# Performance work log

Hardware: AMD Instinct MI355X
Metric: run time of the kernel (lower is better)

Reference implementation:

```python
import jax, jax.numpy as jnp
import numpy as np

T = 128        # number of timesteps (init arg T)
LEN_M = 32     # causal window length (init arg len_M)
N = 8192       # nodes
F = 64         # features per node


def setup_inputs() -> dict:
    key = jax.random.key(0)
    k1, k2, k3 = jax.random.split(key, 3)
    X = jax.random.normal(k1, (T, N, F), dtype=jnp.float32)
    # M_pad[r] holds the length-(r+1) parameter M[str(r+1)] in its first r+1 slots
    # (padding is masked out before softmax, so its values are irrelevant).
    M_pad = jax.random.normal(k2, (LEN_M, LEN_M), dtype=jnp.float32)
    # M_big[j] corresponds to parameter key str(LEN_M+1+j); keys LEN_M+1..T-1 are
    # used by rows LEN_M+1..T-1 (row LEN_M reuses M[str(LEN_M)] = M_pad[-1], per the source).
    M_big = jax.random.normal(k3, (T - LEN_M - 1, LEN_M), dtype=jnp.float32)
    return {"X": X, "M_pad": M_pad, "M_big": M_big}


def _band_weights(M_pad, M_big):
    """Build the [T, T] causal banded mixing matrix with per-row softmax weights."""
    cols = jnp.arange(LEN_M)
    # rows 0..LEN_M-1: softmax over the growing prefix window of length row+1
    prefix_mask = cols[None, :] <= jnp.arange(LEN_M)[:, None]            # [LEN_M, LEN_M]
    w_small = jax.nn.softmax(jnp.where(prefix_mask, M_pad, -jnp.inf), axis=1)
    # rows LEN_M..T-1 use key str(row): row==LEN_M reuses M_pad[-1], rest use M_big
    logits_big = jnp.concatenate([M_pad[LEN_M - 1:LEN_M], M_big], axis=0)  # [T-LEN_M, LEN_M]
    w_big = jax.nn.softmax(logits_big, axis=1)
    W = jnp.zeros((T, T), dtype=M_pad.dtype)
    W = W.at[:LEN_M, :LEN_M].set(w_small)  # w_small is zero outside the prefix window
    rows = jnp.arange(LEN_M, T)
    cidx = (rows - LEN_M + 1)[:, None] + cols[None, :]  # sliding window cols per row
    W = W.at[rows[:, None], cidx].set(w_big)
    return W


def reference(X, M_pad, M_big):
    W = _band_weights(M_pad, M_big)          # [T, T] banded
    data = X.reshape(T, -1)                  # [T, N*F]
    out = W @ data                           # causal windowed weighted sum, all rows at once
    return out.reshape(X.shape)
```

## Files before the change

kernel.cpp:

```cpp
#include <hip/hip_runtime.h>
#include <math.h>

#define T_    128
#define LENM  32
#define NCOL  (8192 * 64)

typedef float f4_t __attribute__((ext_vector_type(4)));

__global__ void build_w_kernel(const float* __restrict__ M_pad,
                               const float* __restrict__ M_big,
                               float* __restrict__ Wc) {
    int t = threadIdx.x;
    if (t >= T_) return;
    const float* src;
    int len, joff;
    if (t < LENM)       { src = M_pad + t * LENM;              len = t + 1; joff = LENM - 1 - t; }
    else if (t == LENM) { src = M_pad + (LENM - 1) * LENM;     len = LENM;  joff = 0; }
    else                { src = M_big + (t - LENM - 1) * LENM; len = LENM;  joff = 0; }

    float m = -3.4e38f;
    for (int j = 0; j < len; ++j) m = fmaxf(m, src[j]);
    float e[LENM];
    float s = 0.f;
    for (int j = 0; j < len; ++j) { e[j] = expf(src[j] - m); s += e[j]; }
    float inv = 1.f / s;
    for (int j = 0; j < LENM; ++j) Wc[t * LENM + j] = 0.f;
    for (int j = 0; j < len; ++j)  Wc[t * LENM + joff + j] = e[j] * inv;
}

template<int R>
__device__ __forceinline__ void step(const f4_t* __restrict__ xp,
                                     f4_t* __restrict__ op,
                                     const f4_t* w4,
                                     f4_t (&A)[LENM], f4_t (&B)[LENM]) {
    constexpr int K     = R / LENM;
    constexpr int i_    = R % LENM;
    constexpr int jmin_ = (R < LENM) ? (LENM - 1 - i_) : 0;
    f4_t (&CUR)[LENM] = (K & 1) ? B : A;
    f4_t (&PRV)[LENM] = (K & 1) ? A : B;
    const size_t rs = NCOL / 4;

    if constexpr (R + 8 < T_) {
        f4_t ld = xp[(size_t)(R + 8) * rs];
        if constexpr (i_ < LENM - 8) CUR[i_ + 8] = ld;
        else                         PRV[i_ - (LENM - 8)] = ld;
    }

    f4_t acc; acc.x = 0.f; acc.y = 0.f; acc.z = 0.f; acc.w = 0.f;
#pragma unroll
    for (int q = 0; q < 8; ++q) {
        if (q * 4 + 3 >= jmin_) {
            f4_t w = w4[R * 8 + q];
#pragma unroll
            for (int m = 0; m < 4; ++m) {
                const int j = q * 4 + m;
                if (j >= jmin_) {
                    f4_t xv = (j < LENM - 1 - i_) ? PRV[i_ + 1 + j]
                                                  : CUR[i_ + j - (LENM - 1)];
                    float wm = (m == 0) ? w.x : (m == 1) ? w.y
                             : (m == 2) ? w.z : w.w;
                    acc.x = fmaf(wm, xv.x, acc.x);
                    acc.y = fmaf(wm, xv.y, acc.y);
                    acc.z = fmaf(wm, xv.z, acc.z);
                    acc.w = fmaf(wm, xv.w, acc.w);
                }
            }
        }
    }
    __builtin_nontemporal_store(acc, &op[(size_t)R * rs]);
}

template<int R>
__device__ __forceinline__ void run_steps(const f4_t* __restrict__ xp,
                                          f4_t* __restrict__ op,
                                          const f4_t* w4,
                                          f4_t (&A)[LENM], f4_t (&B)[LENM]) {
    if constexpr (R < T_) {
        step<R>(xp, op, w4, A, B);
        run_steps<R + 1>(xp, op, w4, A, B);
    }
}

__global__ __launch_bounds__(256, 2) void band_mix_kernel(
    const float* __restrict__ X,
    const float* __restrict__ Wc,
    float* __restrict__ out) {
    __shared__ f4_t w4[T_ * LENM / 4];
    for (int i = threadIdx.x; i < T_ * LENM / 4; i += 256)
        w4[i] = reinterpret_cast<const f4_t*>(Wc)[i];
    __syncthreads();

    const int c = (blockIdx.x * 256 + threadIdx.x) * 4;
    const f4_t* xp = reinterpret_cast<const f4_t*>(X + c);
    f4_t* op = reinterpret_cast<f4_t*>(out + c);
    const size_t rs = NCOL / 4;

    f4_t A[LENM], B[LENM];
#pragma unroll
    for (int i = 0; i < 8; ++i) A[i] = xp[(size_t)i * rs];

    run_steps<0>(xp, op, w4, A, B);
}

extern "C" void kernel_launch(void* const* d_in, const int* in_sizes, int n_in,
                              void* d_out, int out_size, void* d_ws, size_t ws_size,
                              hipStream_t stream) {
    const float* X     = (const float*)d_in[0];
    const float* M_pad = (const float*)d_in[1];
    const float* M_big = (const float*)d_in[2];
    float* out = (float*)d_out;
    float* Wc  = (float*)d_ws;

    build_w_kernel<<<1, 128, 0, stream>>>(M_pad, M_big, Wc);
    band_mix_kernel<<<NCOL / 4 / 256, 256, 0, stream>>>(X, Wc, out);
}
```

Baseline: 95.32 us.

## Replace double-bank row buffer with 48-slot ring and grouped prefetch

Replaces the two 32-entry register banks with a single 48-slot ring buffer indexed by row modulo 48. Rows are loaded in groups of eight, one group ahead of the group being computed, and a scheduling barrier separates the loads from the FMA work. This keeps more loads in flight and cuts the register footprint of the window. The ring stays large enough that no row still needed is overwritten, but the compiler may reorder or spill registers differently.

After: 106.6 us. 1.12x slower.

```diff
diff --git a/kernel.cpp b/kernel.cpp
--- a/kernel.cpp
+++ b/kernel.cpp
@@ -1,9 +1,11 @@
 #include <hip/hip_runtime.h>
 #include <math.h>
 
-#define T_    128
-#define LENM  32
-#define NCOL  (8192 * 64)
+#define T_     128
+#define LENM   32
+#define NCOL   (8192 * 64)
+#define WSLOTS 48
+#define GRP    8
 
 typedef float f4_t __attribute__((ext_vector_type(4)));
 
@@ -28,35 +30,37 @@
     for (int j = 0; j < len; ++j)  Wc[t * LENM + joff + j] = e[j] * inv;
 }
 
-template<int R>
-__device__ __forceinline__ void step(const f4_t* __restrict__ xp,
-                                     f4_t* __restrict__ op,
-                                     const f4_t* w4,
-                                     f4_t (&A)[LENM], f4_t (&B)[LENM]) {
-    constexpr int K     = R / LENM;
-    constexpr int i_    = R % LENM;
-    constexpr int jmin_ = (R < LENM) ? (LENM - 1 - i_) : 0;
-    f4_t (&CUR)[LENM] = (K & 1) ? B : A;
-    f4_t (&PRV)[LENM] = (K & 1) ? A : B;
-    const size_t rs = NCOL / 4;
 
-    if constexpr (R + 8 < T_) {
-        f4_t ld = xp[(size_t)(R + 8) * rs];
-        if constexpr (i_ < LENM - 8) CUR[i_ + 8] = ld;
-        else                         PRV[i_ - (LENM - 8)] = ld;
+template<int ROW>
+__device__ __forceinline__ void load_row(const f4_t* __restrict__ xp,
+                                         f4_t (&WIN)[WSLOTS]) {
+    WIN[ROW % WSLOTS] = xp[(size_t)ROW * (NCOL / 4)];
+}
+
+template<int R0, int CNT>
+__device__ __forceinline__ void load_rows(const f4_t* __restrict__ xp,
+                                          f4_t (&WIN)[WSLOTS]) {
+    if constexpr (CNT > 0) {
+        load_row<R0>(xp, WIN);
+        load_rows<R0 + 1, CNT - 1>(xp, WIN);
     }
+}
 
+template<int ROW>
+__device__ __forceinline__ void compute_row(f4_t* __restrict__ op,
+                                            const f4_t* w4,
+                                            const f4_t (&WIN)[WSLOTS]) {
+    constexpr int jmin_ = (ROW < LENM) ? (LENM - 1 - ROW) : 0;
     f4_t acc; acc.x = 0.f; acc.y = 0.f; acc.z = 0.f; acc.w = 0.f;
 #pragma unroll
     for (int q = 0; q < 8; ++q) {
         if (q * 4 + 3 >= jmin_) {
-            f4_t w = w4[R * 8 + q];
+            f4_t w = w4[ROW * 8 + q];
 #pragma unroll
             for (int m = 0; m < 4; ++m) {
                 const int j = q * 4 + m;
                 if (j >= jmin_) {
-                    f4_t xv = (j < LENM - 1 - i_) ? PRV[i_ + 1 + j]
-                                                  : CUR[i_ + j - (LENM - 1)];
+                    f4_t xv = WIN[(ROW - (LENM - 1) + j) % WSLOTS];
                     float wm = (m == 0) ? w.x : (m == 1) ? w.y
                              : (m == 2) ? w.z : w.w;
                     acc.x = fmaf(wm, xv.x, acc.x);
@@ -67,17 +71,38 @@
             }
         }
     }
-    __builtin_nontemporal_store(acc, &op[(size_t)R * rs]);
+    __builtin_nontemporal_store(acc, &op[(size_t)ROW * (NCOL / 4)]);
 }
 
-template<int R>
-__device__ __forceinline__ void run_steps(const f4_t* __restrict__ xp,
-                                          f4_t* __restrict__ op,
-                                          const f4_t* w4,
-                                          f4_t (&A)[LENM], f4_t (&B)[LENM]) {
-    if constexpr (R < T_) {
-        step<R>(xp, op, w4, A, B);
-        run_steps<R + 1>(xp, op, w4, A, B);
+template<int R0, int CNT>
+__device__ __forceinline__ void compute_rows(f4_t* __restrict__ op,
+                                             const f4_t* w4,
+                                             const f4_t (&WIN)[WSLOTS]) {
+    if constexpr (CNT > 0) {
+        compute_row<R0>(op, w4, WIN);
+        compute_rows<R0 + 1, CNT - 1>(op, w4, WIN);
+    }
+}
+
+template<int G>
+__device__ __forceinline__ void do_group(const f4_t* __restrict__ xp,
+                                         f4_t* __restrict__ op,
+                                         const f4_t* w4,
+                                         f4_t (&WIN)[WSLOTS]) {
+    if constexpr (G * GRP + GRP < T_)
+        load_rows<G * GRP + GRP, GRP>(xp, WIN);
+    __builtin_amdgcn_sched_barrier(0);
+    compute_rows<G * GRP, GRP>(op, w4, WIN);
+}
+
+template<int G>
+__device__ __forceinline__ void run_groups(const f4_t* __restrict__ xp,
+                                           f4_t* __restrict__ op,
+                                           const f4_t* w4,
+                                           f4_t (&WIN)[WSLOTS]) {
+    if constexpr (G * GRP < T_) {
+        do_group<G>(xp, op, w4, WIN);
+        run_groups<G + 1>(xp, op, w4, WIN);
     }
 }
 
@@ -93,13 +118,11 @@
     const int c = (blockIdx.x * 256 + threadIdx.x) * 4;
     const f4_t* xp = reinterpret_cast<const f4_t*>(X + c);
     f4_t* op = reinterpret_cast<f4_t*>(out + c);
-    const size_t rs = NCOL / 4;
 
-    f4_t A[LENM], B[LENM];
-#pragma unroll
-    for (int i = 0; i < 8; ++i) A[i] = xp[(size_t)i * rs];
+    f4_t WIN[WSLOTS];
+    load_rows<0, GRP>(xp, WIN);
 
-    run_steps<0>(xp, op, w4, A, B);
+    run_groups<0>(xp, op, w4, WIN);
 }
 
 extern "C" void kernel_launch(void* const* d_in, const int* in_sizes, int n_in,
```
